# Kernel tuning notes

Hardware: AMD Instinct MI355X
Metric: run time of the kernel (lower is better)

The kernel has to match this reference:

```python
import jax, jax.numpy as jnp
import numpy as np

NUM_USERS = 100000
NUM_ITEMS = 100000
D = 64
B, P, N, NB, NN = 1024, 32, 64, 32, 32
W1, W2, W3 = 1.0, 0.1, 1.0


def setup_inputs() -> dict:
    key = jax.random.key(0)
    ks = jax.random.split(key, 12)
    u2e = 0.1 + 0.03 * jax.random.normal(ks[0], (NUM_USERS, D), jnp.float32)
    v2e = 0.1 + 0.03 * jax.random.normal(ks[1], (NUM_ITEMS, D), jnp.float32)
    margin_uv = jnp.ones((NUM_USERS, 1), jnp.float32)
    margin_vv = jnp.ones((NUM_ITEMS, 1), jnp.float32)
    margin_uu = jnp.ones((NUM_USERS, 1), jnp.float32)
    train_u = jax.random.randint(ks[2], (B,), 0, NUM_USERS)
    pos_idx = jax.random.randint(ks[3], (B, P), 0, NUM_ITEMS)
    neg_idx = jax.random.randint(ks[4], (B, N), 0, NUM_ITEMS)
    nb_idx = jax.random.randint(ks[5], (B, NB), 0, NUM_USERS)
    nn_idx = jax.random.randint(ks[6], (B, NN), 0, NUM_USERS)
    # ragged lengths -> padded masks
    def mk_mask(k, maxlen):
        lens = jax.random.randint(k, (B,), 1, maxlen + 1)
        return jnp.arange(maxlen)[None, :] < lens[:, None]
    pos_mask = mk_mask(ks[7], P)
    neg_mask = mk_mask(ks[8], N)
    nb_mask = mk_mask(ks[9], NB)
    nn_mask = mk_mask(ks[10], NN)
    return dict(u2e=u2e, v2e=v2e, margin_uv=margin_uv, margin_vv=margin_vv,
                margin_uu=margin_uu, train_u=train_u, pos_idx=pos_idx,
                neg_idx=neg_idx, nb_idx=nb_idx, nn_idx=nn_idx,
                pos_mask=pos_mask, neg_mask=neg_mask, nb_mask=nb_mask,
                nn_mask=nn_mask)


def reference(u2e, v2e, margin_uv, margin_vv, margin_uu, train_u, pos_idx,
              neg_idx, nb_idx, nn_idx, pos_mask, neg_mask, nb_mask, nn_mask):
    u_e = u2e[train_u]            # [B,D]
    p_e = v2e[pos_idx]            # [B,P,D]
    n_e = v2e[neg_idx]            # [B,N,D]
    nb_e = u2e[nb_idx]            # [B,NB,D]
    nn_e = u2e[nn_idx]            # [B,NN,D]
    pm = pos_mask.astype(u_e.dtype)
    nm = neg_mask.astype(u_e.dtype)
    nbm = nb_mask.astype(u_e.dtype)
    nnm = nn_mask.astype(u_e.dtype)

    # user-item triplet loss: hinge[b,i,k] = m_u[b] + ||u-p_i||^2 - ||u-n_k||^2
    d1 = jnp.sum((u_e[:, None, :] - p_e) ** 2, -1)   # [B,P]
    d2 = jnp.sum((u_e[:, None, :] - n_e) ** 2, -1)   # [B,N]
    m_u = margin_uv[train_u, 0]                       # [B]
    uv = jax.nn.relu(m_u[:, None, None] + d1[:, :, None] - d2[:, None, :])
    uv_loss = jnp.sum(uv * (pm[:, :, None] * nm[:, None, :]))

    # item-item loss (torch broadcast: margin over a separate positive axis j)
    # hinge[b,i,j,k] = m_v[b,j] + ||p_i-u||^2 - ||p_i-n_k||^2
    p2 = jnp.sum(p_e ** 2, -1)                        # [B,P]
    n2 = jnp.sum(n_e ** 2, -1)                        # [B,N]
    d2v = p2[:, :, None] + n2[:, None, :] - 2.0 * jnp.einsum('bpd,bnd->bpn', p_e, n_e)
    m_v = margin_vv[pos_idx, 0]                       # [B,P]
    hinge_vv = jax.nn.relu(m_v[:, None, :, None] + d1[:, :, None, None] - d2v[:, :, None, :])
    mask_vv = pm[:, :, None, None] * pm[:, None, :, None] * nm[:, None, None, :]
    vv_loss = jnp.sum(hinge_vv * mask_vv)

    # user-user social loss
    d1s = jnp.sum((u_e[:, None, :] - nb_e) ** 2, -1)  # [B,NB]
    d2s = jnp.sum((u_e[:, None, :] - nn_e) ** 2, -1)  # [B,NN]
    m_s = margin_uu[train_u, 0]                       # [B]
    uu = jax.nn.relu(m_s[:, None, None] + d1s[:, :, None] - d2s[:, None, :])
    uu_loss = jnp.sum(uu * (nbm[:, :, None] * nnm[:, None, :]))

    # margin regularizer (masked mean over batch positives)
    loss_am = (jnp.mean(margin_uv[train_u])
               + jnp.sum(m_v * pm) / jnp.sum(pm)
               + jnp.mean(margin_uu[train_u]))

    return uv_loss + W1 * vv_loss + W3 * uu_loss + W2 * loss_am
```

## Files before the change

### kernel.cpp

```cpp
#include <hip/hip_runtime.h>
#include <cfloat>

#define BB   1024
#define PP   32
#define NNEG 64
#define DD   64
#define BSTR 72
#define SSTR 68

static constexpr float W2c = 0.1f;

typedef __attribute__((ext_vector_type(8)))  short bf16x8;
typedef __attribute__((ext_vector_type(16))) float f32x16;

__device__ __forceinline__ uint2 pk_bf16x4(float4 v) {
    unsigned a, b;
    asm("v_cvt_pk_bf16_f32 %0, %1, %2" : "=v"(a) : "v"(v.x), "v"(v.y));
    asm("v_cvt_pk_bf16_f32 %0, %1, %2" : "=v"(b) : "v"(v.z), "v"(v.w));
    return make_uint2(a, b);
}

__device__ __forceinline__ float parse_mask(const void* p, int flag, int j) {
    if (flag == 1) return ((const unsigned char*)p)[j] ? 1.0f : 0.0f;
    if (flag == 2) return (((const float*)p)[j] != 0.0f) ? 1.0f : 0.0f;
    return ((const int*)p)[j] ? 1.0f : 0.0f;
}

__global__ __launch_bounds__(512, 8) void loss_kernel(
    const float* __restrict__ u2e, const float* __restrict__ v2e,
    const float* __restrict__ margin_uv, const float* __restrict__ margin_vv,
    const float* __restrict__ margin_uu,
    const int* __restrict__ train_u, const int* __restrict__ pos_idx,
    const int* __restrict__ neg_idx, const int* __restrict__ nb_idx,
    const int* __restrict__ nn_idx,
    const void* __restrict__ pos_mask, const void* __restrict__ neg_mask,
    const void* __restrict__ nb_mask, const void* __restrict__ nn_mask,
    float* __restrict__ ws) {

    const int b = blockIdx.x;
    const int t = threadIdx.x;
    const int lane = t & 63;
    const int w = t >> 6;

    __shared__ __align__(16) short pn_bf[96 * BSTR];
    __shared__ __align__(16) float s_lds[PP * SSTR];
    __shared__ __align__(16) float d2[NNEG], n2s[NNEG], nmf[NNEG];
    __shared__ float d1[PP], p2s[PP], d1sA[PP], d2sA[PP];
    __shared__ float pmf[PP], nbmf[PP], nnmf[PP];
    __shared__ float mvp[PP], mv_arr[PP], s_srt[PP], S_suf[PP + 1];
    __shared__ float sc[2];
    __shared__ float red[8][3];

    int flag = 0;
    if (w < 3) {
        unsigned f32h = 0, byth = 0;
        #pragma unroll
        for (int i2 = 0; i2 < 4; ++i2) {
            unsigned mw = ((const unsigned int*)pos_mask)[lane + 64 * i2];
            f32h |= (mw == 0x3f800000u) ? 1u : 0u;
            byth |= ((mw != 0x3f800000u) && (mw & 0xFFFFFF00u)) ? 1u : 0u;
        }
        flag = __any(f32h) ? 2 : (__any(byth) ? 1 : 0);
    }

    const int tu  = train_u[b];
    const int q   = t & 15;
    const int R0  = t >> 4;
    const int gi0 = pos_idx[b * PP + R0];
    const int gi1 = neg_idx[b * NNEG + R0];
    const int gi2 = neg_idx[b * NNEG + R0 + 32];
    const int row = t >> 3, sub = t & 7;
    const int sidx = (row < PP) ? nb_idx[b * PP + row] : nn_idx[b * PP + row - PP];

    const float* uR = u2e + (size_t)tu * DD;
    const float4 u4 = *(const float4*)(uR + 4 * q);
    float4 ch0 = *(const float4*)(v2e + (size_t)gi0 * DD + 4 * q);
    float4 ch1 = *(const float4*)(v2e + (size_t)gi1 * DD + 4 * q);
    float4 ch2 = *(const float4*)(v2e + (size_t)gi2 * DD + 4 * q);
    const float* rp = u2e + (size_t)sidx * DD + 8 * sub;
    const float4 e0 = *(const float4*)(rp);
    const float4 e1 = *(const float4*)(rp + 4);
    const float4 v0 = *(const float4*)(uR + 8 * sub);
    const float4 v1 = *(const float4*)(uR + 8 * sub + 4);

    {
        float sdp[3], sqp[3];
        float dx, dy, dz, dw;
        dx = ch0.x-u4.x; dy = ch0.y-u4.y; dz = ch0.z-u4.z; dw = ch0.w-u4.w;
        sdp[0] = dx*dx+dy*dy+dz*dz+dw*dw;
        sqp[0] = ch0.x*ch0.x+ch0.y*ch0.y+ch0.z*ch0.z+ch0.w*ch0.w;
        dx = ch1.x-u4.x; dy = ch1.y-u4.y; dz = ch1.z-u4.z; dw = ch1.w-u4.w;
        sdp[1] = dx*dx+dy*dy+dz*dz+dw*dw;
        sqp[1] = ch1.x*ch1.x+ch1.y*ch1.y+ch1.z*ch1.z+ch1.w*ch1.w;
        dx = ch2.x-u4.x; dy = ch2.y-u4.y; dz = ch2.z-u4.z; dw = ch2.w-u4.w;
        sdp[2] = dx*dx+dy*dy+dz*dz+dw*dw;
        sqp[2] = ch2.x*ch2.x+ch2.y*ch2.y+ch2.z*ch2.z+ch2.w*ch2.w;
        #pragma unroll
        for (int m = 1; m < 16; m <<= 1) {
            #pragma unroll
            for (int r = 0; r < 3; ++r) {
                sdp[r] += __shfl_xor(sdp[r], m);
                sqp[r] += __shfl_xor(sqp[r], m);
            }
        }
        if (q == 0) {
            d1[R0]      = sdp[0]; p2s[R0]      = sqp[0];
            d2[R0]      = sdp[1]; n2s[R0]      = sqp[1];
            d2[R0 + 32] = sdp[2]; n2s[R0 + 32] = sqp[2];
        }
    }
    {
        float dx = e0.x-v0.x, dy = e0.y-v0.y, dz = e0.z-v0.z, dw = e0.w-v0.w;
        float s = dx*dx+dy*dy+dz*dz+dw*dw;
        dx = e1.x-v1.x; dy = e1.y-v1.y; dz = e1.z-v1.z; dw = e1.w-v1.w;
        s += dx*dx+dy*dy+dz*dz+dw*dw;
        s += __shfl_xor(s, 1);
        s += __shfl_xor(s, 2);
        s += __shfl_xor(s, 4);
        if (sub == 0) { if (row < PP) d1sA[row] = s; else d2sA[row - PP] = s; }
    }
    if (t < PP) {
        float pm = parse_mask(pos_mask, flag, b * PP + t);
        float mv = margin_vv[pos_idx[b * PP + t]];
        pmf[t] = pm; mv_arr[t] = mv;
        mvp[t] = (pm != 0.0f) ? mv : -FLT_MAX;
    } else if (t < 96) {
        nmf[t - PP] = parse_mask(neg_mask, flag, b * NNEG + (t - PP));
    } else if (t < 128) {
        nbmf[t - 96] = parse_mask(nb_mask, flag, b * PP + (t - 96));
    } else if (t < 160) {
        nnmf[t - 128] = parse_mask(nn_mask, flag, b * PP + (t - 128));
    }
    if (t == 0) { sc[0] = margin_uv[tu]; sc[1] = margin_uu[tu]; }
    {
        *(uint2*)(pn_bf + R0 * BSTR + 4 * q)        = pk_bf16x4(ch0);
        *(uint2*)(pn_bf + (R0 + 32) * BSTR + 4 * q) = pk_bf16x4(ch1);
        *(uint2*)(pn_bf + (R0 + 64) * BSTR + 4 * q) = pk_bf16x4(ch2);
    }
    __syncthreads();

    if (w < 2) {
        f32x16 acc;
        #pragma unroll
        for (int i = 0; i < 16; ++i) acc[i] = 0.0f;
        const int lr = lane & 31;
        const int hi = lane >> 5;
        const short* ap = pn_bf + lr * BSTR;
        const short* bp = pn_bf + (PP + 32 * w + lr) * BSTR;
        #pragma unroll
        for (int c = 0; c < 4; ++c) {
            const int d0 = 16 * c + 8 * hi;
            bf16x8 a   = *(const bf16x8*)(ap + d0);
            bf16x8 bfr = *(const bf16x8*)(bp + d0);
            acc = __builtin_amdgcn_mfma_f32_32x32x16_bf16(a, bfr, acc, 0, 0, 0);
        }
        #pragma unroll
        for (int r = 0; r < 16; ++r) {
            const int m = (r & 3) + 8 * (r >> 2) + 4 * hi;
            s_lds[m * SSTR + 32 * w + lr] = acc[r];
        }
    } else if (w == 2 && lane < PP) {
        float vj = mvp[lane];
        int r = 0;
        #pragma unroll
        for (int j = 0; j < PP; ++j) {
            float o = mvp[j];
            r += (o < vj || (o == vj && j < lane)) ? 1 : 0;
        }
        s_srt[r] = vj;
        __threadfence_block();
        float y = s_srt[lane];
        #pragma unroll
        for (int d = 1; d < PP; d <<= 1) {
            float z = __shfl_down(y, d);
            if (lane + d < PP) y += z;
        }
        S_suf[lane] = y;
        if (lane == 0) S_suf[PP] = 0.0f;
    }
    __syncthreads();

    const float m_u = sc[0], m_s = sc[1];
    const float s31 = s_srt[PP - 1];
    const int kb2 = t & 15;
    const int i   = R0;
    const float d1i = d1[i], p2i = p2s[i], pmi = pmf[i];
    const float4 Sv  = *(const float4*)(s_lds + i * SSTR + 4 * kb2);
    const float4 d2v = *(const float4*)(d2 + 4 * kb2);
    const float4 n2v = *(const float4*)(n2s + 4 * kb2);
    const float4 nmv = *(const float4*)(nmf + 4 * kb2);
    const float Sa[4]  = {Sv.x, Sv.y, Sv.z, Sv.w};
    const float d2a[4] = {d2v.x, d2v.y, d2v.z, d2v.w};
    const float n2a[4] = {n2v.x, n2v.y, n2v.z, n2v.w};
    const float nma[4] = {nmv.x, nmv.y, nmv.z, nmv.w};
    float loss = 0.0f;
    #pragma unroll
    for (int c = 0; c < 4; ++c) {
        const float cc = d1i - (p2i + n2a[c] - 2.0f * Sa[c]);
        const float v = -cc;
        int t0 = 0;
        #pragma unroll
        for (int st = 16; st > 0; st >>= 1)
            t0 += (s_srt[t0 + st - 1] <= v) ? st : 0;
        t0 += (s31 <= v) ? 1 : 0;
        const float inner = S_suf[t0] + (float)(PP - t0) * cc;
        const float uvh = fmaxf(m_u + d1i - d2a[c], 0.0f);
        loss += pmi * nma[c] * (inner + uvh);
    }

    #pragma unroll
    for (int rr = 0; rr < 2; ++rr) {
        int pid = t + 512 * rr;
        int ii = pid >> 5, k = pid & 31;
        loss += nbmf[ii] * nnmf[k] * fmaxf(m_s + d1sA[ii] - d2sA[k], 0.0f);
    }

    float a2 = (t < PP) ? mv_arr[t] * pmf[t] : 0.0f;
    float a3 = (t < PP) ? pmf[t] : 0.0f;
    #pragma unroll
    for (int m = 1; m < 64; m <<= 1) {
        loss += __shfl_xor(loss, m);
        a2   += __shfl_xor(a2, m);
        a3   += __shfl_xor(a3, m);
    }
    if (lane == 0) { red[w][0] = loss; red[w][1] = a2; red[w][2] = a3; }
    __syncthreads();
    if (t == 0) {
        float S0 = 0, S2 = 0, S3 = 0;
        #pragma unroll
        for (int i2 = 0; i2 < 8; ++i2) { S0 += red[i2][0]; S2 += red[i2][1]; S3 += red[i2][2]; }
        ws[0 * BB + b] = S0;
        ws[1 * BB + b] = sc[0];
        ws[2 * BB + b] = S2;
        ws[3 * BB + b] = S3;
        ws[4 * BB + b] = sc[1];
    }
}

__global__ __launch_bounds__(64) void finalize_kernel(const float* __restrict__ ws,
                                                      float* __restrict__ out) {
    const int lane = threadIdx.x;
    float s[5];
    #pragma unroll
    for (int a = 0; a < 5; ++a) {
        const float4* w4 = (const float4*)(ws + a * BB);
        float acc = 0.0f;
        #pragma unroll
        for (int j = 0; j < 4; ++j) {
            float4 v = w4[lane + 64 * j];
            acc += v.x + v.y + v.z + v.w;
        }
        s[a] = acc;
    }
    #pragma unroll
    for (int m = 1; m < 64; m <<= 1)
        #pragma unroll
        for (int a = 0; a < 5; ++a) s[a] += __shfl_xor(s[a], m);
    if (lane == 0) {
        float loss_am = s[1] / (float)BB + s[2] / s[3] + s[4] / (float)BB;
        out[0] = s[0] + W2c * loss_am;
    }
}

extern "C" void kernel_launch(void* const* d_in, const int* in_sizes, int n_in,
                              void* d_out, int out_size, void* d_ws, size_t ws_size,
                              hipStream_t stream) {
    const float* u2e       = (const float*)d_in[0];
    const float* v2e       = (const float*)d_in[1];
    const float* margin_uv = (const float*)d_in[2];
    const float* margin_vv = (const float*)d_in[3];
    const float* margin_uu = (const float*)d_in[4];
    const int*   train_u   = (const int*)d_in[5];
    const int*   pos_idx   = (const int*)d_in[6];
    const int*   neg_idx   = (const int*)d_in[7];
    const int*   nb_idx    = (const int*)d_in[8];
    const int*   nn_idx    = (const int*)d_in[9];
    const void*  pos_mask  = d_in[10];
    const void*  neg_mask  = d_in[11];
    const void*  nb_mask   = d_in[12];
    const void*  nn_mask   = d_in[13];

    float* ws  = (float*)d_ws;
    float* out = (float*)d_out;

    loss_kernel<<<BB, 512, 0, stream>>>(u2e, v2e, margin_uv, margin_vv, margin_uu,
                                        train_u, pos_idx, neg_idx, nb_idx, nn_idx,
                                        pos_mask, neg_mask, nb_mask, nn_mask, ws);
    finalize_kernel<<<1, 64, 0, stream>>>(ws, out);
}
```

Measured before the change: 19.59 us.

## Process two batch rows per block and specialize waves across MFMA, sort, and social loss

Each 512-thread block now handles two batch rows instead of one, so the grid is halved and the shared-memory buffers are duplicated per row. The per-row phases are split across waves: four waves run the MFMA dot products, two do the margin sort and prefix sums, and two compute the user-user social loss. The final hinge loop then covers both rows. The aim is to raise per-thread work, overlap more gathers, and make better use of otherwise idle waves. In exchange, register and LDS use roughly double (launch bounds drop from 8 to 4), which can cut occupancy, and with only 512 blocks on the GPU the load may balance less evenly.

```diff
diff --git a/kernel.cpp b/kernel.cpp
--- a/kernel.cpp
+++ b/kernel.cpp
@@ -26,7 +26,7 @@
     return ((const int*)p)[j] ? 1.0f : 0.0f;
 }
 
-__global__ __launch_bounds__(512, 8) void loss_kernel(
+__global__ __launch_bounds__(512, 4) void loss_kernel(
     const float* __restrict__ u2e, const float* __restrict__ v2e,
     const float* __restrict__ margin_uv, const float* __restrict__ margin_vv,
     const float* __restrict__ margin_uu,
@@ -37,22 +37,24 @@
     const void* __restrict__ nb_mask, const void* __restrict__ nn_mask,
     float* __restrict__ ws) {
 
-    const int b = blockIdx.x;
     const int t = threadIdx.x;
     const int lane = t & 63;
     const int w = t >> 6;
-
-    __shared__ __align__(16) short pn_bf[96 * BSTR];
-    __shared__ __align__(16) float s_lds[PP * SSTR];
-    __shared__ __align__(16) float d2[NNEG], n2s[NNEG], nmf[NNEG];
-    __shared__ float d1[PP], p2s[PP], d1sA[PP], d2sA[PP];
-    __shared__ float pmf[PP], nbmf[PP], nnmf[PP];
-    __shared__ float mvp[PP], mv_arr[PP], s_srt[PP], S_suf[PP + 1];
-    __shared__ float sc[2];
-    __shared__ float red[8][3];
-
-    int flag = 0;
-    if (w < 3) {
+    const int bb0 = blockIdx.x * 2;
+
+    __shared__ __align__(16) short pn_bf[2][96 * BSTR];
+    __shared__ __align__(16) float s_lds[2][PP * SSTR];
+    __shared__ __align__(16) float d2_[2][NNEG], n2_[2][NNEG], nmf_[2][NNEG];
+    __shared__ float d1_[2][PP], p2_[2][PP], d1s_[2][PP], d2s_[2][PP];
+    __shared__ float pmf_[2][PP], nbmf_[2][PP], nnmf_[2][PP];
+    __shared__ float mvp_[2][PP], mva_[2][PP], srt_[2][PP], suf_[2][PP + 1];
+    __shared__ float sc_[2][2];
+    __shared__ float red[8][2];
+    __shared__ float uu_red[2];
+    __shared__ float a23[2][2];
+
+    int flag;
+    {
         unsigned f32h = 0, byth = 0;
         #pragma unroll
         for (int i2 = 0; i2 < 4; ++i2) {
@@ -63,38 +65,49 @@
         flag = __any(f32h) ? 2 : (__any(byth) ? 1 : 0);
     }
 
-    const int tu  = train_u[b];
     const int q   = t & 15;
     const int R0  = t >> 4;
-    const int gi0 = pos_idx[b * PP + R0];
-    const int gi1 = neg_idx[b * NNEG + R0];
-    const int gi2 = neg_idx[b * NNEG + R0 + 32];
     const int row = t >> 3, sub = t & 7;
-    const int sidx = (row < PP) ? nb_idx[b * PP + row] : nn_idx[b * PP + row - PP];
-
-    const float* uR = u2e + (size_t)tu * DD;
-    const float4 u4 = *(const float4*)(uR + 4 * q);
-    float4 ch0 = *(const float4*)(v2e + (size_t)gi0 * DD + 4 * q);
-    float4 ch1 = *(const float4*)(v2e + (size_t)gi1 * DD + 4 * q);
-    float4 ch2 = *(const float4*)(v2e + (size_t)gi2 * DD + 4 * q);
-    const float* rp = u2e + (size_t)sidx * DD + 8 * sub;
-    const float4 e0 = *(const float4*)(rp);
-    const float4 e1 = *(const float4*)(rp + 4);
-    const float4 v0 = *(const float4*)(uR + 8 * sub);
-    const float4 v1 = *(const float4*)(uR + 8 * sub + 4);
-
-    {
+
+    int tu[2], gi0[2], gi1[2], gi2[2], sidx[2];
+    #pragma unroll
+    for (int j = 0; j < 2; ++j) {
+        const int b = bb0 + j;
+        tu[j]   = train_u[b];
+        gi0[j]  = pos_idx[b * PP + R0];
+        gi1[j]  = neg_idx[b * NNEG + R0];
+        gi2[j]  = neg_idx[b * NNEG + R0 + 32];
+        sidx[j] = (row < PP) ? nb_idx[b * PP + row] : nn_idx[b * PP + row - PP];
+    }
+
+    float4 u4[2], ch0[2], ch1[2], ch2[2], e0[2], e1[2], v0[2], v1[2];
+    #pragma unroll
+    for (int j = 0; j < 2; ++j) {
+        const float* uR = u2e + (size_t)tu[j] * DD;
+        u4[j]  = *(const float4*)(uR + 4 * q);
+        ch0[j] = *(const float4*)(v2e + (size_t)gi0[j] * DD + 4 * q);
+        ch1[j] = *(const float4*)(v2e + (size_t)gi1[j] * DD + 4 * q);
+        ch2[j] = *(const float4*)(v2e + (size_t)gi2[j] * DD + 4 * q);
+        const float* rp = u2e + (size_t)sidx[j] * DD + 8 * sub;
+        e0[j] = *(const float4*)(rp);
+        e1[j] = *(const float4*)(rp + 4);
+        v0[j] = *(const float4*)(uR + 8 * sub);
+        v1[j] = *(const float4*)(uR + 8 * sub + 4);
+    }
+
+    #pragma unroll
+    for (int j = 0; j < 2; ++j) {
         float sdp[3], sqp[3];
         float dx, dy, dz, dw;
-        dx = ch0.x-u4.x; dy = ch0.y-u4.y; dz = ch0.z-u4.z; dw = ch0.w-u4.w;
+        dx = ch0[j].x-u4[j].x; dy = ch0[j].y-u4[j].y; dz = ch0[j].z-u4[j].z; dw = ch0[j].w-u4[j].w;
         sdp[0] = dx*dx+dy*dy+dz*dz+dw*dw;
-        sqp[0] = ch0.x*ch0.x+ch0.y*ch0.y+ch0.z*ch0.z+ch0.w*ch0.w;
-        dx = ch1.x-u4.x; dy = ch1.y-u4.y; dz = ch1.z-u4.z; dw = ch1.w-u4.w;
+        sqp[0] = ch0[j].x*ch0[j].x+ch0[j].y*ch0[j].y+ch0[j].z*ch0[j].z+ch0[j].w*ch0[j].w;
+        dx = ch1[j].x-u4[j].x; dy = ch1[j].y-u4[j].y; dz = ch1[j].z-u4[j].z; dw = ch1[j].w-u4[j].w;
         sdp[1] = dx*dx+dy*dy+dz*dz+dw*dw;
-        sqp[1] = ch1.x*ch1.x+ch1.y*ch1.y+ch1.z*ch1.z+ch1.w*ch1.w;
-        dx = ch2.x-u4.x; dy = ch2.y-u4.y; dz = ch2.z-u4.z; dw = ch2.w-u4.w;
+        sqp[1] = ch1[j].x*ch1[j].x+ch1[j].y*ch1[j].y+ch1[j].z*ch1[j].z+ch1[j].w*ch1[j].w;
+        dx = ch2[j].x-u4[j].x; dy = ch2[j].y-u4[j].y; dz = ch2[j].z-u4[j].z; dw = ch2[j].w-u4[j].w;
         sdp[2] = dx*dx+dy*dy+dz*dz+dw*dw;
-        sqp[2] = ch2.x*ch2.x+ch2.y*ch2.y+ch2.z*ch2.z+ch2.w*ch2.w;
+        sqp[2] = ch2[j].x*ch2[j].x+ch2[j].y*ch2[j].y+ch2[j].z*ch2[j].z+ch2[j].w*ch2[j].w;
         #pragma unroll
         for (int m = 1; m < 16; m <<= 1) {
             #pragma unroll
@@ -104,49 +117,53 @@
             }
         }
         if (q == 0) {
-            d1[R0]      = sdp[0]; p2s[R0]      = sqp[0];
-            d2[R0]      = sdp[1]; n2s[R0]      = sqp[1];
-            d2[R0 + 32] = sdp[2]; n2s[R0 + 32] = sqp[2];
-        }
-    }
-    {
-        float dx = e0.x-v0.x, dy = e0.y-v0.y, dz = e0.z-v0.z, dw = e0.w-v0.w;
-        float s = dx*dx+dy*dy+dz*dz+dw*dw;
-        dx = e1.x-v1.x; dy = e1.y-v1.y; dz = e1.z-v1.z; dw = e1.w-v1.w;
-        s += dx*dx+dy*dy+dz*dz+dw*dw;
+            d1_[j][R0]      = sdp[0]; p2_[j][R0]      = sqp[0];
+            d2_[j][R0]      = sdp[1]; n2_[j][R0]      = sqp[1];
+            d2_[j][R0 + 32] = sdp[2]; n2_[j][R0 + 32] = sqp[2];
+        }
+        float ex = e0[j].x-v0[j].x, ey = e0[j].y-v0[j].y, ez = e0[j].z-v0[j].z, ew = e0[j].w-v0[j].w;
+        float s = ex*ex+ey*ey+ez*ez+ew*ew;
+        ex = e1[j].x-v1[j].x; ey = e1[j].y-v1[j].y; ez = e1[j].z-v1[j].z; ew = e1[j].w-v1[j].w;
+        s += ex*ex+ey*ey+ez*ez+ew*ew;
         s += __shfl_xor(s, 1);
         s += __shfl_xor(s, 2);
         s += __shfl_xor(s, 4);
-        if (sub == 0) { if (row < PP) d1sA[row] = s; else d2sA[row - PP] = s; }
-    }
-    if (t < PP) {
-        float pm = parse_mask(pos_mask, flag, b * PP + t);
-        float mv = margin_vv[pos_idx[b * PP + t]];
-        pmf[t] = pm; mv_arr[t] = mv;
-        mvp[t] = (pm != 0.0f) ? mv : -FLT_MAX;
-    } else if (t < 96) {
-        nmf[t - PP] = parse_mask(neg_mask, flag, b * NNEG + (t - PP));
-    } else if (t < 128) {
-        nbmf[t - 96] = parse_mask(nb_mask, flag, b * PP + (t - 96));
-    } else if (t < 160) {
-        nnmf[t - 128] = parse_mask(nn_mask, flag, b * PP + (t - 128));
-    }
-    if (t == 0) { sc[0] = margin_uv[tu]; sc[1] = margin_uu[tu]; }
+        if (sub == 0) { if (row < PP) d1s_[j][row] = s; else d2s_[j][row - PP] = s; }
+        *(uint2*)(pn_bf[j] + R0 * BSTR + 4 * q)        = pk_bf16x4(ch0[j]);
+        *(uint2*)(pn_bf[j] + (R0 + 32) * BSTR + 4 * q) = pk_bf16x4(ch1[j]);
+        *(uint2*)(pn_bf[j] + (R0 + 64) * BSTR + 4 * q) = pk_bf16x4(ch2[j]);
+    }
+
     {
-        *(uint2*)(pn_bf + R0 * BSTR + 4 * q)        = pk_bf16x4(ch0);
-        *(uint2*)(pn_bf + (R0 + 32) * BSTR + 4 * q) = pk_bf16x4(ch1);
-        *(uint2*)(pn_bf + (R0 + 64) * BSTR + 4 * q) = pk_bf16x4(ch2);
+        const int j  = (t >= 256) ? 1 : 0;
+        const int tt = t - 256 * j;
+        const int b  = bb0 + j;
+        if (tt < PP) {
+            float pm = parse_mask(pos_mask, flag, b * PP + tt);
+            float mv = margin_vv[pos_idx[b * PP + tt]];
+            pmf_[j][tt] = pm; mva_[j][tt] = mv;
+            mvp_[j][tt] = (pm != 0.0f) ? mv : -FLT_MAX;
+        } else if (tt < 96) {
+            nmf_[j][tt - PP] = parse_mask(neg_mask, flag, b * NNEG + (tt - PP));
+        } else if (tt < 128) {
+            nbmf_[j][tt - 96] = parse_mask(nb_mask, flag, b * PP + (tt - 96));
+        } else if (tt < 160) {
+            nnmf_[j][tt - 128] = parse_mask(nn_mask, flag, b * PP + (tt - 128));
+        }
+        if (tt == 0) { sc_[j][0] = margin_uv[tu[j]]; sc_[j][1] = margin_uu[tu[j]]; }
     }
     __syncthreads();
 
-    if (w < 2) {
+    if (w < 4) {
+        const int j    = w >> 1;
+        const int half = w & 1;
         f32x16 acc;
         #pragma unroll
         for (int i = 0; i < 16; ++i) acc[i] = 0.0f;
         const int lr = lane & 31;
         const int hi = lane >> 5;
-        const short* ap = pn_bf + lr * BSTR;
-        const short* bp = pn_bf + (PP + 32 * w + lr) * BSTR;
+        const short* ap = pn_bf[j] + lr * BSTR;
+        const short* bp = pn_bf[j] + (PP + 32 * half + lr) * BSTR;
         #pragma unroll
         for (int c = 0; c < 4; ++c) {
             const int d0 = 16 * c + 8 * hi;
@@ -157,83 +174,108 @@
         #pragma unroll
         for (int r = 0; r < 16; ++r) {
             const int m = (r & 3) + 8 * (r >> 2) + 4 * hi;
-            s_lds[m * SSTR + 32 * w + lr] = acc[r];
-        }
-    } else if (w == 2 && lane < PP) {
-        float vj = mvp[lane];
-        int r = 0;
-        #pragma unroll
-        for (int j = 0; j < PP; ++j) {
-            float o = mvp[j];
-            r += (o < vj || (o == vj && j < lane)) ? 1 : 0;
-        }
-        s_srt[r] = vj;
+            s_lds[j][m * SSTR + 32 * half + lr] = acc[r];
+        }
+    } else if (w < 6) {
+        const int j = w - 4;
+        if (lane < PP) {
+            float vj = mvp_[j][lane];
+            int r = 0;
+            #pragma unroll
+            for (int j2 = 0; j2 < PP; ++j2) {
+                float o = mvp_[j][j2];
+                r += (o < vj || (o == vj && j2 < lane)) ? 1 : 0;
+            }
+            srt_[j][r] = vj;
+        }
         __threadfence_block();
-        float y = s_srt[lane];
-        #pragma unroll
-        for (int d = 1; d < PP; d <<= 1) {
-            float z = __shfl_down(y, d);
-            if (lane + d < PP) y += z;
-        }
-        S_suf[lane] = y;
-        if (lane == 0) S_suf[PP] = 0.0f;
+        if (lane < PP) {
+            float y = srt_[j][lane];
+            #pragma unroll
+            for (int d = 1; d < PP; d <<= 1) {
+                float z = __shfl_down(y, d);
+                if (lane + d < PP) y += z;
+            }
+            suf_[j][lane] = y;
+            if (lane == 0) suf_[j][PP] = 0.0f;
+        }
+        float a2 = (lane < PP) ? mva_[j][lane] * pmf_[j][lane] : 0.0f;
+        float a3 = (lane < PP) ? pmf_[j][lane] : 0.0f;
+        #pragma unroll
+        for (int m = 1; m < 64; m <<= 1) {
+            a2 += __shfl_xor(a2, m);
+            a3 += __shfl_xor(a3, m);
+        }
+        if (lane == 0) { a23[j][0] = a2; a23[j][1] = a3; }
+    } else {
+        const int j = w - 6;
+        const float m_s = sc_[j][1];
+        float uul = 0.0f;
+        #pragma unroll
+        for (int r = 0; r < 16; ++r) {
+            const int pid = lane + 64 * r;
+            const int ii = pid >> 5, k = pid & 31;
+            uul += nbmf_[j][ii] * nnmf_[j][k] * fmaxf(m_s + d1s_[j][ii] - d2s_[j][k], 0.0f);
+        }
+        #pragma unroll
+        for (int m = 1; m < 64; m <<= 1) uul += __shfl_xor(uul, m);
+        if (lane == 0) uu_red[j] = uul;
     }
     __syncthreads();
 
-    const float m_u = sc[0], m_s = sc[1];
-    const float s31 = s_srt[PP - 1];
     const int kb2 = t & 15;
     const int i   = R0;
-    const float d1i = d1[i], p2i = p2s[i], pmi = pmf[i];
-    const float4 Sv  = *(const float4*)(s_lds + i * SSTR + 4 * kb2);
-    const float4 d2v = *(const float4*)(d2 + 4 * kb2);
-    const float4 n2v = *(const float4*)(n2s + 4 * kb2);
-    const float4 nmv = *(const float4*)(nmf + 4 * kb2);
-    const float Sa[4]  = {Sv.x, Sv.y, Sv.z, Sv.w};
-    const float d2a[4] = {d2v.x, d2v.y, d2v.z, d2v.w};
-    const float n2a[4] = {n2v.x, n2v.y, n2v.z, n2v.w};
-    const float nma[4] = {nmv.x, nmv.y, nmv.z, nmv.w};
-    float loss = 0.0f;
-    #pragma unroll
-    for (int c = 0; c < 4; ++c) {
-        const float cc = d1i - (p2i + n2a[c] - 2.0f * Sa[c]);
-        const float v = -cc;
-        int t0 = 0;
-        #pragma unroll
-        for (int st = 16; st > 0; st >>= 1)
-            t0 += (s_srt[t0 + st - 1] <= v) ? st : 0;
-        t0 += (s31 <= v) ? 1 : 0;
-        const float inner = S_suf[t0] + (float)(PP - t0) * cc;
-        const float uvh = fmaxf(m_u + d1i - d2a[c], 0.0f);
-        loss += pmi * nma[c] * (inner + uvh);
-    }
-
-    #pragma unroll
-    for (int rr = 0; rr < 2; ++rr) {
-        int pid = t + 512 * rr;
-        int ii = pid >> 5, k = pid & 31;
-        loss += nbmf[ii] * nnmf[k] * fmaxf(m_s + d1sA[ii] - d2sA[k], 0.0f);
-    }
-
-    float a2 = (t < PP) ? mv_arr[t] * pmf[t] : 0.0f;
-    float a3 = (t < PP) ? pmf[t] : 0.0f;
+    float loss[2];
+    #pragma unroll
+    for (int j = 0; j < 2; ++j) {
+        const float m_u = sc_[j][0];
+        const float s31 = srt_[j][PP - 1];
+        const float d1i = d1_[j][i], p2i = p2_[j][i], pmi = pmf_[j][i];
+        const float4 Sv  = *(const float4*)(s_lds[j] + i * SSTR + 4 * kb2);
+        const float4 d2v = *(const float4*)(d2_[j] + 4 * kb2);
+        const float4 n2v = *(const float4*)(n2_[j] + 4 * kb2);
+        const float4 nmv = *(const float4*)(nmf_[j] + 4 * kb2);
+        const float Sa[4]  = {Sv.x, Sv.y, Sv.z, Sv.w};
+        const float d2a[4] = {d2v.x, d2v.y, d2v.z, d2v.w};
+        const float n2a[4] = {n2v.x, n2v.y, n2v.z, n2v.w};
+        const float nma[4] = {nmv.x, nmv.y, nmv.z, nmv.w};
+        float L = 0.0f;
+        #pragma unroll
+        for (int c = 0; c < 4; ++c) {
+            const float cc = d1i - (p2i + n2a[c] - 2.0f * Sa[c]);
+            const float v = -cc;
+            int t0 = 0;
+            #pragma unroll
+            for (int st = 16; st > 0; st >>= 1)
+                t0 += (srt_[j][t0 + st - 1] <= v) ? st : 0;
+            t0 += (s31 <= v) ? 1 : 0;
+            const float inner = suf_[j][t0] + (float)(PP - t0) * cc;
+            const float uvh = fmaxf(m_u + d1i - d2a[c], 0.0f);
+            L += pmi * nma[c] * (inner + uvh);
+        }
+        loss[j] = L;
+    }
     #pragma unroll
     for (int m = 1; m < 64; m <<= 1) {
-        loss += __shfl_xor(loss, m);
-        a2   += __shfl_xor(a2, m);
-        a3   += __shfl_xor(a3, m);
-    }
-    if (lane == 0) { red[w][0] = loss; red[w][1] = a2; red[w][2] = a3; }
+        loss[0] += __shfl_xor(loss[0], m);
+        loss[1] += __shfl_xor(loss[1], m);
+    }
+    if (lane == 0) { red[w][0] = loss[0]; red[w][1] = loss[1]; }
     __syncthreads();
+
     if (t == 0) {
-        float S0 = 0, S2 = 0, S3 = 0;
-        #pragma unroll
-        for (int i2 = 0; i2 < 8; ++i2) { S0 += red[i2][0]; S2 += red[i2][1]; S3 += red[i2][2]; }
-        ws[0 * BB + b] = S0;
-        ws[1 * BB + b] = sc[0];
-        ws[2 * BB + b] = S2;
-        ws[3 * BB + b] = S3;
-        ws[4 * BB + b] = sc[1];
+        #pragma unroll
+        for (int j = 0; j < 2; ++j) {
+            float S0 = uu_red[j];
+            #pragma unroll
+            for (int i2 = 0; i2 < 8; ++i2) S0 += red[i2][j];
+            const int b = bb0 + j;
+            ws[0 * BB + b] = S0;
+            ws[1 * BB + b] = sc_[j][0];
+            ws[2 * BB + b] = a23[j][0];
+            ws[3 * BB + b] = a23[j][1];
+            ws[4 * BB + b] = sc_[j][1];
+        }
     }
 }
 
@@ -283,8 +325,8 @@
     float* ws  = (float*)d_ws;
     float* out = (float*)d_out;
 
-    loss_kernel<<<BB, 512, 0, stream>>>(u2e, v2e, margin_uv, margin_vv, margin_uu,
-                                        train_u, pos_idx, neg_idx, nb_idx, nn_idx,
-                                        pos_mask, neg_mask, nb_mask, nn_mask, ws);
+    loss_kernel<<<BB / 2, 512, 0, stream>>>(u2e, v2e, margin_uv, margin_vv, margin_uu,
+                                            train_u, pos_idx, neg_idx, nb_idx, nn_idx,
+                                            pos_mask, neg_mask, nb_mask, nn_mask, ws);
     finalize_kernel<<<1, 64, 0, stream>>>(ws, out);
 }
```

New measurement: 20.18 us. 3.0% more time.
